# Performance work log

Measured on AMD Instinct MI355X. Metric: run time of the kernel, lower is better.

Reference implementation:

```python
import jax, jax.numpy as jnp
import numpy as np

T, K, H, B = 4096, 64, 128, 128


def setup_inputs() -> dict:
    key = jax.random.key(0)
    ks = jax.random.split(key, 6)
    stdv = 1.0 / np.sqrt(H)  # matches init_weights_random: uniform(-stdv, stdv)
    x = jax.random.normal(ks[0], (T, K, B), dtype=jnp.float32)
    init_hidden_states = jax.random.normal(ks[1], (H, B), dtype=jnp.float32)
    A1 = jax.random.uniform(ks[2], (K, K), minval=-stdv, maxval=stdv, dtype=jnp.float32)
    A2 = jax.random.uniform(ks[3], (K, H), minval=-stdv, maxval=stdv, dtype=jnp.float32)
    A3 = jax.random.uniform(ks[4], (H, K), minval=-stdv, maxval=stdv, dtype=jnp.float32)
    A4 = jax.random.uniform(ks[5], (H, H), minval=-stdv, maxval=stdv, dtype=jnp.float32)
    return {"x": x, "init_hidden_states": init_hidden_states,
            "A1": A1, "A2": A2, "A3": A3, "A4": A4}


def reference(x, init_hidden_states, A1, A2, A3, A4):
    # x: [T, K, B]; hidden: [H, B]
    # known_t = A1 @ x_t + A2 @ h_{t-1};  h_t = A3 @ x_t + A4 @ h_{t-1}
    def step(h, x_t):
        known = A1 @ x_t + A2 @ h
        h_new = A3 @ x_t + A4 @ h
        return h_new, (known, h_new)

    _, (known_seq, hidden_seq) = jax.lax.scan(step, init_hidden_states, x)
    return known_seq, hidden_seq  # [T, K, B], [T, H, B]
```

## Files before the change

kernel.cpp:

```cpp
#include <hip/hip_runtime.h>
#include <stdint.h>

typedef _Float16 half8 __attribute__((ext_vector_type(8)));
typedef float floatx4 __attribute__((ext_vector_type(4)));

constexpr int T  = 4096;
constexpr int KD = 64;
constexpr int HD = 128;
constexpr int BD = 128;
constexpr int KT = KD + HD;
constexpr int CH = 64;
constexpr int LS = T / CH;
constexpr int BC = 32;
constexpr int NSP = BD / BC;

static_assert(CH * LS == T, "");

constexpr size_t W_OFF = 0;
constexpr size_t M_OFF = 73728;
constexpr size_t U_OFF = 131072;
constexpr size_t S_OFF = U_OFF + (size_t)CH * HD * BD * 4;

__device__ __forceinline__ unsigned short f2h(float v) {
  _Float16 h = (_Float16)v;
  return __builtin_bit_cast(unsigned short, h);
}
__device__ __forceinline__ unsigned pack2(float a, float b) {
  return (unsigned)f2h(a) | ((unsigned)f2h(b) << 16);
}
__device__ __forceinline__ int swz(int g, int n) {
  return (g & ~7) | ((g & 7) ^ (n & 7));
}

__global__ __launch_bounds__(256) void prep_kernel(
    const float* __restrict__ A1, const float* __restrict__ A2,
    const float* __restrict__ A3, const float* __restrict__ A4,
    unsigned short* __restrict__ Wf, unsigned short* __restrict__ Mf) {
  if (blockIdx.x < 36) {
    for (int e = 0; e < 4; ++e) {
      int id = blockIdx.x * 1024 + e * 256 + threadIdx.x;
      int r = id / KT, cc = id % KT;
      float v;
      if (r < KD) v = (cc < KD) ? A1[r * KD + cc] : A2[r * HD + (cc - KD)];
      else        v = (cc < KD) ? A3[(r - KD) * KD + cc] : A4[(r - KD) * HD + (cc - KD)];
      Wf[id] = f2h(v);
    }
    return;
  }
  __shared__ __align__(16) unsigned short Mrow[HD * HD];
  __shared__ __align__(16) unsigned short Mcol[HD * HD];
  const int tid = threadIdx.x;
  for (int j = 0; j < 64; ++j) {
    int id = j * 256 + tid;
    int r = id >> 7, cc = id & 127;
    unsigned short hb = f2h(A4[id]);
    Mrow[id] = hb;
    Mcol[cc * HD + r] = hb;
  }
  __syncthreads();
  const int wv = tid >> 6, ln = tid & 63, l15 = ln & 15, q = ln >> 4;
  for (int it = 0; it < 6; ++it) {
    half8 af[2][4];
#pragma unroll
    for (int m = 0; m < 2; ++m)
#pragma unroll
      for (int kt = 0; kt < 4; ++kt)
        af[m][kt] = *reinterpret_cast<const half8*>(
            &Mrow[(wv * 32 + m * 16 + l15) * HD + kt * 32 + q * 8]);
    floatx4 acc[2][8];
#pragma unroll
    for (int m = 0; m < 2; ++m)
#pragma unroll
      for (int nt = 0; nt < 8; ++nt) {
        floatx4 z = {0.f, 0.f, 0.f, 0.f};
        acc[m][nt] = z;
      }
#pragma unroll
    for (int kt = 0; kt < 4; ++kt)
#pragma unroll
      for (int nt = 0; nt < 8; ++nt) {
        half8 bf = *reinterpret_cast<const half8*>(
            &Mcol[(nt * 16 + l15) * HD + kt * 32 + q * 8]);
#pragma unroll
        for (int m = 0; m < 2; ++m)
          acc[m][nt] = __builtin_amdgcn_mfma_f32_16x16x32_f16(af[m][kt], bf, acc[m][nt], 0, 0, 0);
      }
    __syncthreads();
#pragma unroll
    for (int m = 0; m < 2; ++m)
#pragma unroll
      for (int nt = 0; nt < 8; ++nt) {
        int Rb = wv * 32 + m * 16 + q * 4;
        int col = nt * 16 + l15;
#pragma unroll
        for (int r = 0; r < 4; ++r) {
          unsigned short hb = f2h(acc[m][nt][r]);
          Mrow[(Rb + r) * HD + col] = hb;
          Mcol[col * HD + (Rb + r)] = hb;
        }
      }
    __syncthreads();
  }
  for (int j = 0; j < 64; ++j) {
    int id = j * 256 + tid;
    Mf[id] = Mrow[id];
  }
}

template <bool WRITE_OUT, bool ZERO_INIT>
__global__ __launch_bounds__(256) void rnn_pass(
    const float* __restrict__ x, const unsigned short* __restrict__ Wf,
    const float* __restrict__ init_h, const float* __restrict__ s_buf,
    float* __restrict__ u_out, float* __restrict__ out_known,
    float* __restrict__ out_hidden) {
  const int c = blockIdx.x / NSP;
  const int col0 = (blockIdx.x % NSP) * BC;
  const int tid = threadIdx.x;
  const int wv = tid >> 6;
  const int ln = tid & 63;
  const int l15 = ln & 15;
  const int q = ln >> 4;

  __shared__ __align__(16) unsigned short Bsh[BC * KT];

  half8 afrag[3][6];
#pragma unroll
  for (int m = 0; m < 3; ++m)
#pragma unroll
    for (int kt = 0; kt < 6; ++kt)
      afrag[m][kt] = *reinterpret_cast<const half8*>(
          Wf + (wv * 48 + m * 16 + l15) * KT + kt * 32 + q * 8);

  {
    const float* hsrc = nullptr;
    if (!ZERO_INIT) hsrc = (c == 0) ? init_h : (s_buf + (size_t)c * HD * BD);
    int b = tid & 31;
    int r0 = (tid >> 5) * 16;
    float hv[16];
#pragma unroll
    for (int j = 0; j < 16; ++j)
      hv[j] = hsrc ? hsrc[(size_t)(r0 + j) * BD + col0 + b] : 0.f;
#pragma unroll
    for (int hf = 0; hf < 2; ++hf) {
      int o = hf * 8;
      uint4 v;
      v.x = pack2(hv[o + 0], hv[o + 1]);
      v.y = pack2(hv[o + 2], hv[o + 3]);
      v.z = pack2(hv[o + 4], hv[o + 5]);
      v.w = pack2(hv[o + 6], hv[o + 7]);
      int k0 = KD + r0 + o;
      *reinterpret_cast<uint4*>(&Bsh[b * KT + swz(k0 >> 3, b) * 8]) = v;
    }
  }
  {
    int b = tid & 31;
    int k0 = (tid >> 5) * 8;
    const float* xp = x + (size_t)(c * LS) * KD * BD + col0 + b;
    float xv[8];
#pragma unroll
    for (int j = 0; j < 8; ++j) xv[j] = xp[(size_t)(k0 + j) * BD];
    uint4 v;
    v.x = pack2(xv[0], xv[1]);
    v.y = pack2(xv[2], xv[3]);
    v.z = pack2(xv[4], xv[5]);
    v.w = pack2(xv[6], xv[7]);
    *reinterpret_cast<uint4*>(&Bsh[b * KT + swz(k0 >> 3, b) * 8]) = v;
  }
  __syncthreads();

  for (int i = 0; i < LS; ++i) {
    const int t = c * LS + i;
    float xv[8];
    const int b = tid & 31;
    const int xk0 = (tid >> 5) * 8;
    if (i + 1 < LS) {
      const float* xp = x + (size_t)(t + 1) * KD * BD + col0 + b;
#pragma unroll
      for (int j = 0; j < 8; ++j) xv[j] = xp[(size_t)(xk0 + j) * BD];
    }
    floatx4 acc[3][2];
#pragma unroll
    for (int m = 0; m < 3; ++m)
#pragma unroll
      for (int nt = 0; nt < 2; ++nt) {
        floatx4 z = {0.f, 0.f, 0.f, 0.f};
        acc[m][nt] = z;
      }
#pragma unroll
    for (int kt = 0; kt < 6; ++kt)
#pragma unroll
      for (int nt = 0; nt < 2; ++nt) {
        int n = nt * 16 + l15;
        half8 bf = *reinterpret_cast<const half8*>(
            &Bsh[n * KT + swz(kt * 4 + q, n) * 8]);
#pragma unroll
        for (int m = 0; m < 3; ++m)
          acc[m][nt] = __builtin_amdgcn_mfma_f32_16x16x32_f16(
              afrag[m][kt], bf, acc[m][nt], 0, 0, 0);
      }
    __syncthreads();
#pragma unroll
    for (int m = 0; m < 3; ++m) {
      int Rb = wv * 48 + m * 16 + q * 4;
#pragma unroll
      for (int nt = 0; nt < 2; ++nt) {
        int col = col0 + nt * 16 + l15;
        if (Rb < KD) {
          if (WRITE_OUT) {
            float* kp = out_known + (size_t)t * KD * BD + (size_t)Rb * BD + col;
#pragma unroll
            for (int r = 0; r < 4; ++r) kp[(size_t)r * BD] = acc[m][nt][r];
          }
        } else {
          int hr = Rb - KD;
          if (WRITE_OUT) {
            float* hp = out_hidden + (size_t)t * HD * BD + (size_t)hr * BD + col;
#pragma unroll
            for (int r = 0; r < 4; ++r) hp[(size_t)r * BD] = acc[m][nt][r];
          }
          if (!WRITE_OUT && i == LS - 1) {
            float* up = u_out + ((size_t)c * HD + hr) * BD + col;
#pragma unroll
            for (int r = 0; r < 4; ++r) up[(size_t)r * BD] = acc[m][nt][r];
          }
          int n = nt * 16 + l15;
          uint2 pk;
          pk.x = pack2(acc[m][nt][0], acc[m][nt][1]);
          pk.y = pack2(acc[m][nt][2], acc[m][nt][3]);
          *reinterpret_cast<uint2*>(&Bsh[n * KT + swz(Rb >> 3, n) * 8 + (Rb & 7)]) = pk;
        }
      }
    }
    if (i + 1 < LS) {
      uint4 v;
      v.x = pack2(xv[0], xv[1]);
      v.y = pack2(xv[2], xv[3]);
      v.z = pack2(xv[4], xv[5]);
      v.w = pack2(xv[6], xv[7]);
      *reinterpret_cast<uint4*>(&Bsh[b * KT + swz(xk0 >> 3, b) * 8]) = v;
    }
    __syncthreads();
  }
}

__global__ __launch_bounds__(256) void combine_kernel(
    const unsigned short* __restrict__ Mf, const float* __restrict__ init_h,
    const float* __restrict__ u_buf, float* __restrict__ s_buf) {
  const int col0 = blockIdx.x * BC;
  const int tid = threadIdx.x;
  const int wv = tid >> 6;
  const int ln = tid & 63;
  const int l15 = ln & 15;
  const int q = ln >> 4;
  __shared__ __align__(16) unsigned short Hsh[BC * HD];

  half8 af[2][4];
#pragma unroll
  for (int m = 0; m < 2; ++m)
#pragma unroll
    for (int kt = 0; kt < 4; ++kt)
      af[m][kt] = *reinterpret_cast<const half8*>(
          Mf + (wv * 32 + m * 16 + l15) * HD + kt * 32 + q * 8);

  {
    int b = tid & 31;
    int r0 = (tid >> 5) * 16;
    float hv[16];
#pragma unroll
    for (int j = 0; j < 16; ++j)
      hv[j] = init_h[(size_t)(r0 + j) * BD + col0 + b];
#pragma unroll
    for (int hf = 0; hf < 2; ++hf) {
      int o = hf * 8;
      uint4 v;
      v.x = pack2(hv[o + 0], hv[o + 1]);
      v.y = pack2(hv[o + 2], hv[o + 3]);
      v.z = pack2(hv[o + 4], hv[o + 5]);
      v.w = pack2(hv[o + 6], hv[o + 7]);
      *reinterpret_cast<uint4*>(&Hsh[b * HD + swz((r0 + o) >> 3, b) * 8]) = v;
    }
  }
  __syncthreads();

  float ua[2][2][4], ub[2][2][4];
  auto load_u = [&](float(&dst)[2][2][4], int cc) {
    const float* up = u_buf + (size_t)cc * HD * BD;
#pragma unroll
    for (int m = 0; m < 2; ++m) {
      int Rb = wv * 32 + m * 16 + q * 4;
#pragma unroll
      for (int nt = 0; nt < 2; ++nt) {
        int col = col0 + nt * 16 + l15;
#pragma unroll
        for (int r = 0; r < 4; ++r)
          dst[m][nt][r] = up[(size_t)(Rb + r) * BD + col];
      }
    }
  };
  auto stepf = [&](int cc, const float(&uc)[2][2][4]) {
    floatx4 acc[2][2];
#pragma unroll
    for (int m = 0; m < 2; ++m)
#pragma unroll
      for (int nt = 0; nt < 2; ++nt) {
        floatx4 z = {0.f, 0.f, 0.f, 0.f};
        acc[m][nt] = z;
      }
#pragma unroll
    for (int kt = 0; kt < 4; ++kt)
#pragma unroll
      for (int nt = 0; nt < 2; ++nt) {
        int n = nt * 16 + l15;
        half8 bf = *reinterpret_cast<const half8*>(
            &Hsh[n * HD + swz(kt * 4 + q, n) * 8]);
#pragma unroll
        for (int m = 0; m < 2; ++m)
          acc[m][nt] = __builtin_amdgcn_mfma_f32_16x16x32_f16(af[m][kt], bf, acc[m][nt], 0, 0, 0);
      }
    __syncthreads();
#pragma unroll
    for (int m = 0; m < 2; ++m) {
      int Rb = wv * 32 + m * 16 + q * 4;
#pragma unroll
      for (int nt = 0; nt < 2; ++nt) {
        int col = col0 + nt * 16 + l15;
        float s0 = acc[m][nt][0] + uc[m][nt][0];
        float s1 = acc[m][nt][1] + uc[m][nt][1];
        float s2 = acc[m][nt][2] + uc[m][nt][2];
        float s3 = acc[m][nt][3] + uc[m][nt][3];
        float* sp = s_buf + ((size_t)(cc + 1) * HD + Rb) * BD + col;
        sp[0] = s0; sp[BD] = s1; sp[2 * BD] = s2; sp[3 * BD] = s3;
        int n = nt * 16 + l15;
        uint2 pk;
        pk.x = pack2(s0, s1);
        pk.y = pack2(s2, s3);
        *reinterpret_cast<uint2*>(&Hsh[n * HD + swz(Rb >> 3, n) * 8 + (Rb & 7)]) = pk;
      }
    }
    __syncthreads();
  };

  load_u(ua, 0);
  load_u(ub, 1);
  int cc = 0;
  while (cc < CH - 1) {
    stepf(cc, ua);
    if (cc + 2 < CH - 1) load_u(ua, cc + 2);
    ++cc;
    if (cc >= CH - 1) break;
    stepf(cc, ub);
    if (cc + 2 < CH - 1) load_u(ub, cc + 2);
    ++cc;
  }
}

extern "C" void kernel_launch(void* const* d_in, const int* in_sizes, int n_in,
                              void* d_out, int out_size, void* d_ws, size_t ws_size,
                              hipStream_t stream) {
  const float* x  = (const float*)d_in[0];
  const float* ih = (const float*)d_in[1];
  const float* A1 = (const float*)d_in[2];
  const float* A2 = (const float*)d_in[3];
  const float* A3 = (const float*)d_in[4];
  const float* A4 = (const float*)d_in[5];
  char* ws = (char*)d_ws;
  unsigned short* Wf = (unsigned short*)(ws + W_OFF);
  unsigned short* Mf = (unsigned short*)(ws + M_OFF);
  float* u_buf = (float*)(ws + U_OFF);
  float* s_buf = (float*)(ws + S_OFF);
  float* known = (float*)d_out;
  float* hidden = known + (size_t)T * KD * BD;

  prep_kernel<<<37, 256, 0, stream>>>(A1, A2, A3, A4, Wf, Mf);
  rnn_pass<false, true><<<(CH - 1) * NSP, 256, 0, stream>>>(
      x, Wf, nullptr, nullptr, u_buf, nullptr, nullptr);
  combine_kernel<<<NSP, 256, 0, stream>>>(Mf, ih, u_buf, s_buf);
  rnn_pass<true, false><<<CH * NSP, 256, 0, stream>>>(
      x, Wf, ih, s_buf, nullptr, known, hidden);
}
```

Before: 683.7 us.

## Use two-level hierarchical combine with more chunks and fp16 state buffers

Doubles the number of time chunks and replaces the single serial combine over all chunks with a three-stage scheme: grouped aggregation of chunk states, a short serial scan over groups using A4^256, then a parallel fill within groups using A4^32. Chunk-end and start states are stored in fp16 in a batch-major layout, and rnn_pass gets an occupancy hint. This shortens the serial critical path and doubles parallelism in both rnn passes, at the cost of extra kernel launches, higher matrix powers computed in fp16 (accuracy risk), and more rounding of intermediate states.

```diff
diff --git a/kernel.cpp b/kernel.cpp
--- a/kernel.cpp
+++ b/kernel.cpp
@@ -9,22 +9,30 @@
 constexpr int HD = 128;
 constexpr int BD = 128;
 constexpr int KT = KD + HD;
-constexpr int CH = 64;
+constexpr int CH = 128;
 constexpr int LS = T / CH;
 constexpr int BC = 32;
 constexpr int NSP = BD / BC;
+constexpr int G  = 8;
+constexpr int NG = CH / G;
 
 static_assert(CH * LS == T, "");
-
-constexpr size_t W_OFF = 0;
-constexpr size_t M_OFF = 73728;
-constexpr size_t U_OFF = 131072;
-constexpr size_t S_OFF = U_OFF + (size_t)CH * HD * BD * 4;
+static_assert(NG * G == CH, "");
+
+constexpr size_t W_OFF  = 0;
+constexpr size_t M_OFF  = 73728;
+constexpr size_t M8_OFF = M_OFF + 32768;
+constexpr size_t U_OFF  = M8_OFF + 32768;
+constexpr size_t S_OFF  = U_OFF + (size_t)CH * BD * HD * 2;
+constexpr size_t AGG_OFF = S_OFF + (size_t)CH * BD * HD * 2;
 
 __device__ __forceinline__ unsigned short f2h(float v) {
   _Float16 h = (_Float16)v;
   return __builtin_bit_cast(unsigned short, h);
 }
+__device__ __forceinline__ float h2f(unsigned short u) {
+  return (float)__builtin_bit_cast(_Float16, u);
+}
 __device__ __forceinline__ unsigned pack2(float a, float b) {
   return (unsigned)f2h(a) | ((unsigned)f2h(b) << 16);
 }
@@ -35,7 +43,8 @@
 __global__ __launch_bounds__(256) void prep_kernel(
     const float* __restrict__ A1, const float* __restrict__ A2,
     const float* __restrict__ A3, const float* __restrict__ A4,
-    unsigned short* __restrict__ Wf, unsigned short* __restrict__ Mf) {
+    unsigned short* __restrict__ Wf, unsigned short* __restrict__ Mf,
+    unsigned short* __restrict__ M8f) {
   if (blockIdx.x < 36) {
     for (int e = 0; e < 4; ++e) {
       int id = blockIdx.x * 1024 + e * 256 + threadIdx.x;
@@ -59,7 +68,7 @@
   }
   __syncthreads();
   const int wv = tid >> 6, ln = tid & 63, l15 = ln & 15, q = ln >> 4;
-  for (int it = 0; it < 6; ++it) {
+  for (int it = 0; it < 8; ++it) {
     half8 af[2][4];
 #pragma unroll
     for (int m = 0; m < 2; ++m)
@@ -100,18 +109,26 @@
         }
       }
     __syncthreads();
-  }
-  for (int j = 0; j < 64; ++j) {
-    int id = j * 256 + tid;
-    Mf[id] = Mrow[id];
+    if (it == 4) {
+      for (int j = 0; j < 64; ++j) {
+        int id = j * 256 + tid;
+        Mf[id] = Mrow[id];
+      }
+    }
+    if (it == 7) {
+      for (int j = 0; j < 64; ++j) {
+        int id = j * 256 + tid;
+        M8f[id] = Mrow[id];
+      }
+    }
   }
 }
 
 template <bool WRITE_OUT, bool ZERO_INIT>
-__global__ __launch_bounds__(256) void rnn_pass(
+__global__ __launch_bounds__(256, 2) void rnn_pass(
     const float* __restrict__ x, const unsigned short* __restrict__ Wf,
-    const float* __restrict__ init_h, const float* __restrict__ s_buf,
-    float* __restrict__ u_out, float* __restrict__ out_known,
+    const float* __restrict__ init_h, const unsigned short* __restrict__ s16,
+    unsigned short* __restrict__ u16, float* __restrict__ out_known,
     float* __restrict__ out_hidden) {
   const int c = blockIdx.x / NSP;
   const int col0 = (blockIdx.x % NSP) * BC;
@@ -132,24 +149,33 @@
           Wf + (wv * 48 + m * 16 + l15) * KT + kt * 32 + q * 8);
 
   {
-    const float* hsrc = nullptr;
-    if (!ZERO_INIT) hsrc = (c == 0) ? init_h : (s_buf + (size_t)c * HD * BD);
     int b = tid & 31;
     int r0 = (tid >> 5) * 16;
-    float hv[16];
-#pragma unroll
-    for (int j = 0; j < 16; ++j)
-      hv[j] = hsrc ? hsrc[(size_t)(r0 + j) * BD + col0 + b] : 0.f;
-#pragma unroll
-    for (int hf = 0; hf < 2; ++hf) {
-      int o = hf * 8;
-      uint4 v;
-      v.x = pack2(hv[o + 0], hv[o + 1]);
-      v.y = pack2(hv[o + 2], hv[o + 3]);
-      v.z = pack2(hv[o + 4], hv[o + 5]);
-      v.w = pack2(hv[o + 6], hv[o + 7]);
-      int k0 = KD + r0 + o;
-      *reinterpret_cast<uint4*>(&Bsh[b * KT + swz(k0 >> 3, b) * 8]) = v;
+    if (ZERO_INIT) {
+      uint4 z = {0u, 0u, 0u, 0u};
+      *reinterpret_cast<uint4*>(&Bsh[b * KT + swz((KD + r0) >> 3, b) * 8]) = z;
+      *reinterpret_cast<uint4*>(&Bsh[b * KT + swz((KD + r0 + 8) >> 3, b) * 8]) = z;
+    } else if (c == 0) {
+      float hv[16];
+#pragma unroll
+      for (int j = 0; j < 16; ++j)
+        hv[j] = init_h[(size_t)(r0 + j) * BD + col0 + b];
+#pragma unroll
+      for (int hf = 0; hf < 2; ++hf) {
+        int o = hf * 8;
+        uint4 v;
+        v.x = pack2(hv[o + 0], hv[o + 1]);
+        v.y = pack2(hv[o + 2], hv[o + 3]);
+        v.z = pack2(hv[o + 4], hv[o + 5]);
+        v.w = pack2(hv[o + 6], hv[o + 7]);
+        *reinterpret_cast<uint4*>(&Bsh[b * KT + swz((KD + r0 + o) >> 3, b) * 8]) = v;
+      }
+    } else {
+      const unsigned short* sp = s16 + ((size_t)c * BD + col0 + b) * HD + r0;
+      uint4 v0 = *reinterpret_cast<const uint4*>(sp);
+      uint4 v1 = *reinterpret_cast<const uint4*>(sp + 8);
+      *reinterpret_cast<uint4*>(&Bsh[b * KT + swz((KD + r0) >> 3, b) * 8]) = v0;
+      *reinterpret_cast<uint4*>(&Bsh[b * KT + swz((KD + r0 + 8) >> 3, b) * 8]) = v1;
     }
   }
   {
@@ -219,9 +245,11 @@
             for (int r = 0; r < 4; ++r) hp[(size_t)r * BD] = acc[m][nt][r];
           }
           if (!WRITE_OUT && i == LS - 1) {
-            float* up = u_out + ((size_t)c * HD + hr) * BD + col;
-#pragma unroll
-            for (int r = 0; r < 4; ++r) up[(size_t)r * BD] = acc[m][nt][r];
+            unsigned short* up = u16 + ((size_t)c * BD + col) * HD + hr;
+            uint2 pku;
+            pku.x = pack2(acc[m][nt][0], acc[m][nt][1]);
+            pku.y = pack2(acc[m][nt][2], acc[m][nt][3]);
+            *reinterpret_cast<uint2*>(up) = pku;
           }
           int n = nt * 16 + l15;
           uint2 pk;
@@ -243,115 +271,147 @@
   }
 }
 
-__global__ __launch_bounds__(256) void combine_kernel(
-    const unsigned short* __restrict__ Mf, const float* __restrict__ init_h,
-    const float* __restrict__ u_buf, float* __restrict__ s_buf) {
+__device__ __forceinline__ void load_mfrag(const unsigned short* Mp, half8 (&af)[2][4],
+                                           int wv, int l15, int q) {
+#pragma unroll
+  for (int m = 0; m < 2; ++m)
+#pragma unroll
+    for (int kt = 0; kt < 4; ++kt)
+      af[m][kt] = *reinterpret_cast<const half8*>(
+          Mp + (wv * 32 + m * 16 + l15) * HD + kt * 32 + q * 8);
+}
+
+__device__ __forceinline__ void stage_h_f32(const float* __restrict__ hsrc,
+                                            unsigned short* Hsh, int col0, int tid) {
+  int b = tid & 31;
+  int r0 = (tid >> 5) * 16;
+  float hv[16];
+#pragma unroll
+  for (int j = 0; j < 16; ++j)
+    hv[j] = hsrc[(size_t)(r0 + j) * BD + col0 + b];
+#pragma unroll
+  for (int hf = 0; hf < 2; ++hf) {
+    int o = hf * 8;
+    uint4 v;
+    v.x = pack2(hv[o + 0], hv[o + 1]);
+    v.y = pack2(hv[o + 2], hv[o + 3]);
+    v.z = pack2(hv[o + 4], hv[o + 5]);
+    v.w = pack2(hv[o + 6], hv[o + 7]);
+    *reinterpret_cast<uint4*>(&Hsh[b * HD + swz((r0 + o) >> 3, b) * 8]) = v;
+  }
+}
+
+__device__ __forceinline__ void stage_h_f16(const unsigned short* __restrict__ sp16,
+                                            unsigned short* Hsh, int col0, int tid) {
+  int b = tid & 31;
+  int r0 = (tid >> 5) * 16;
+  const unsigned short* sp = sp16 + ((size_t)col0 + b) * HD + r0;
+  uint4 v0 = *reinterpret_cast<const uint4*>(sp);
+  uint4 v1 = *reinterpret_cast<const uint4*>(sp + 8);
+  *reinterpret_cast<uint4*>(&Hsh[b * HD + swz(r0 >> 3, b) * 8]) = v0;
+  *reinterpret_cast<uint4*>(&Hsh[b * HD + swz((r0 + 8) >> 3, b) * 8]) = v1;
+}
+
+template <bool WRITE_S>
+__device__ __forceinline__ void comb_step(
+    const half8 (&af)[2][4], unsigned short* Hsh,
+    const unsigned short* __restrict__ uc, unsigned short* __restrict__ sc,
+    int col0, int wv, int l15, int q) {
+  floatx4 acc[2][2];
+#pragma unroll
+  for (int m = 0; m < 2; ++m)
+#pragma unroll
+    for (int nt = 0; nt < 2; ++nt) {
+      floatx4 z = {0.f, 0.f, 0.f, 0.f};
+      acc[m][nt] = z;
+    }
+#pragma unroll
+  for (int kt = 0; kt < 4; ++kt)
+#pragma unroll
+    for (int nt = 0; nt < 2; ++nt) {
+      int n = nt * 16 + l15;
+      half8 bf = *reinterpret_cast<const half8*>(
+          &Hsh[n * HD + swz(kt * 4 + q, n) * 8]);
+#pragma unroll
+      for (int m = 0; m < 2; ++m)
+        acc[m][nt] = __builtin_amdgcn_mfma_f32_16x16x32_f16(af[m][kt], bf, acc[m][nt], 0, 0, 0);
+    }
+  __syncthreads();
+#pragma unroll
+  for (int m = 0; m < 2; ++m) {
+    int Rb = wv * 32 + m * 16 + q * 4;
+#pragma unroll
+    for (int nt = 0; nt < 2; ++nt) {
+      int col = col0 + nt * 16 + l15;
+      uint2 uv = *reinterpret_cast<const uint2*>(uc + (size_t)col * HD + Rb);
+      float s0 = acc[m][nt][0] + h2f((unsigned short)(uv.x & 0xffff));
+      float s1 = acc[m][nt][1] + h2f((unsigned short)(uv.x >> 16));
+      float s2 = acc[m][nt][2] + h2f((unsigned short)(uv.y & 0xffff));
+      float s3 = acc[m][nt][3] + h2f((unsigned short)(uv.y >> 16));
+      uint2 pk;
+      pk.x = pack2(s0, s1);
+      pk.y = pack2(s2, s3);
+      if (WRITE_S) *reinterpret_cast<uint2*>(sc + (size_t)col * HD + Rb) = pk;
+      int n = nt * 16 + l15;
+      *reinterpret_cast<uint2*>(&Hsh[n * HD + swz(Rb >> 3, n) * 8 + (Rb & 7)]) = pk;
+    }
+  }
+  __syncthreads();
+}
+
+__global__ __launch_bounds__(256) void combine_agg(
+    const unsigned short* __restrict__ Mf, const unsigned short* __restrict__ u16,
+    unsigned short* __restrict__ agg16) {
+  const int j = blockIdx.x / NSP;
+  const int col0 = (blockIdx.x % NSP) * BC;
+  const int tid = threadIdx.x;
+  const int wv = tid >> 6, ln = tid & 63, l15 = ln & 15, q = ln >> 4;
+  __shared__ __align__(16) unsigned short Hsh[BC * HD];
+  half8 af[2][4];
+  load_mfrag(Mf, af, wv, l15, q);
+  for (int jj = tid; jj < BC * HD; jj += 256) Hsh[jj] = 0;
+  __syncthreads();
+  for (int i = 0; i < G; ++i) {
+    const unsigned short* uc = u16 + (size_t)(j * G + i) * BD * HD;
+    if (i == G - 1)
+      comb_step<true>(af, Hsh, uc, agg16 + (size_t)j * BD * HD, col0, wv, l15, q);
+    else
+      comb_step<false>(af, Hsh, uc, nullptr, col0, wv, l15, q);
+  }
+}
+
+__global__ __launch_bounds__(256) void combine_serial(
+    const unsigned short* __restrict__ M8f, const float* __restrict__ init_h,
+    const unsigned short* __restrict__ agg16, unsigned short* __restrict__ s16) {
   const int col0 = blockIdx.x * BC;
   const int tid = threadIdx.x;
-  const int wv = tid >> 6;
-  const int ln = tid & 63;
-  const int l15 = ln & 15;
-  const int q = ln >> 4;
+  const int wv = tid >> 6, ln = tid & 63, l15 = ln & 15, q = ln >> 4;
   __shared__ __align__(16) unsigned short Hsh[BC * HD];
-
   half8 af[2][4];
-#pragma unroll
-  for (int m = 0; m < 2; ++m)
-#pragma unroll
-    for (int kt = 0; kt < 4; ++kt)
-      af[m][kt] = *reinterpret_cast<const half8*>(
-          Mf + (wv * 32 + m * 16 + l15) * HD + kt * 32 + q * 8);
-
-  {
-    int b = tid & 31;
-    int r0 = (tid >> 5) * 16;
-    float hv[16];
-#pragma unroll
-    for (int j = 0; j < 16; ++j)
-      hv[j] = init_h[(size_t)(r0 + j) * BD + col0 + b];
-#pragma unroll
-    for (int hf = 0; hf < 2; ++hf) {
-      int o = hf * 8;
-      uint4 v;
-      v.x = pack2(hv[o + 0], hv[o + 1]);
-      v.y = pack2(hv[o + 2], hv[o + 3]);
-      v.z = pack2(hv[o + 4], hv[o + 5]);
-      v.w = pack2(hv[o + 6], hv[o + 7]);
-      *reinterpret_cast<uint4*>(&Hsh[b * HD + swz((r0 + o) >> 3, b) * 8]) = v;
-    }
-  }
-  __syncthreads();
-
-  float ua[2][2][4], ub[2][2][4];
-  auto load_u = [&](float(&dst)[2][2][4], int cc) {
-    const float* up = u_buf + (size_t)cc * HD * BD;
-#pragma unroll
-    for (int m = 0; m < 2; ++m) {
-      int Rb = wv * 32 + m * 16 + q * 4;
-#pragma unroll
-      for (int nt = 0; nt < 2; ++nt) {
-        int col = col0 + nt * 16 + l15;
-#pragma unroll
-        for (int r = 0; r < 4; ++r)
-          dst[m][nt][r] = up[(size_t)(Rb + r) * BD + col];
-      }
-    }
-  };
-  auto stepf = [&](int cc, const float(&uc)[2][2][4]) {
-    floatx4 acc[2][2];
-#pragma unroll
-    for (int m = 0; m < 2; ++m)
-#pragma unroll
-      for (int nt = 0; nt < 2; ++nt) {
-        floatx4 z = {0.f, 0.f, 0.f, 0.f};
-        acc[m][nt] = z;
-      }
-#pragma unroll
-    for (int kt = 0; kt < 4; ++kt)
-#pragma unroll
-      for (int nt = 0; nt < 2; ++nt) {
-        int n = nt * 16 + l15;
-        half8 bf = *reinterpret_cast<const half8*>(
-            &Hsh[n * HD + swz(kt * 4 + q, n) * 8]);
-#pragma unroll
-        for (int m = 0; m < 2; ++m)
-          acc[m][nt] = __builtin_amdgcn_mfma_f32_16x16x32_f16(af[m][kt], bf, acc[m][nt], 0, 0, 0);
-      }
-    __syncthreads();
-#pragma unroll
-    for (int m = 0; m < 2; ++m) {
-      int Rb = wv * 32 + m * 16 + q * 4;
-#pragma unroll
-      for (int nt = 0; nt < 2; ++nt) {
-        int col = col0 + nt * 16 + l15;
-        float s0 = acc[m][nt][0] + uc[m][nt][0];
-        float s1 = acc[m][nt][1] + uc[m][nt][1];
-        float s2 = acc[m][nt][2] + uc[m][nt][2];
-        float s3 = acc[m][nt][3] + uc[m][nt][3];
-        float* sp = s_buf + ((size_t)(cc + 1) * HD + Rb) * BD + col;
-        sp[0] = s0; sp[BD] = s1; sp[2 * BD] = s2; sp[3 * BD] = s3;
-        int n = nt * 16 + l15;
-        uint2 pk;
-        pk.x = pack2(s0, s1);
-        pk.y = pack2(s2, s3);
-        *reinterpret_cast<uint2*>(&Hsh[n * HD + swz(Rb >> 3, n) * 8 + (Rb & 7)]) = pk;
-      }
-    }
-    __syncthreads();
-  };
-
-  load_u(ua, 0);
-  load_u(ub, 1);
-  int cc = 0;
-  while (cc < CH - 1) {
-    stepf(cc, ua);
-    if (cc + 2 < CH - 1) load_u(ua, cc + 2);
-    ++cc;
-    if (cc >= CH - 1) break;
-    stepf(cc, ub);
-    if (cc + 2 < CH - 1) load_u(ub, cc + 2);
-    ++cc;
-  }
+  load_mfrag(M8f, af, wv, l15, q);
+  stage_h_f32(init_h, Hsh, col0, tid);
+  __syncthreads();
+  for (int j = 0; j < NG - 1; ++j)
+    comb_step<true>(af, Hsh, agg16 + (size_t)j * BD * HD,
+                    s16 + (size_t)(j + 1) * G * BD * HD, col0, wv, l15, q);
+}
+
+__global__ __launch_bounds__(256) void combine_fill(
+    const unsigned short* __restrict__ Mf, const float* __restrict__ init_h,
+    const unsigned short* __restrict__ u16, unsigned short* __restrict__ s16) {
+  const int j = blockIdx.x / NSP;
+  const int col0 = (blockIdx.x % NSP) * BC;
+  const int tid = threadIdx.x;
+  const int wv = tid >> 6, ln = tid & 63, l15 = ln & 15, q = ln >> 4;
+  __shared__ __align__(16) unsigned short Hsh[BC * HD];
+  half8 af[2][4];
+  load_mfrag(Mf, af, wv, l15, q);
+  if (j == 0) stage_h_f32(init_h, Hsh, col0, tid);
+  else        stage_h_f16(s16 + (size_t)j * G * BD * HD, Hsh, col0, tid);
+  __syncthreads();
+  for (int i = 0; i < G - 1; ++i)
+    comb_step<true>(af, Hsh, u16 + (size_t)(j * G + i) * BD * HD,
+                    s16 + (size_t)(j * G + i + 1) * BD * HD, col0, wv, l15, q);
 }
 
 extern "C" void kernel_launch(void* const* d_in, const int* in_sizes, int n_in,
@@ -364,17 +424,21 @@
   const float* A3 = (const float*)d_in[4];
   const float* A4 = (const float*)d_in[5];
   char* ws = (char*)d_ws;
-  unsigned short* Wf = (unsigned short*)(ws + W_OFF);
-  unsigned short* Mf = (unsigned short*)(ws + M_OFF);
-  float* u_buf = (float*)(ws + U_OFF);
-  float* s_buf = (float*)(ws + S_OFF);
+  unsigned short* Wf  = (unsigned short*)(ws + W_OFF);
+  unsigned short* Mf  = (unsigned short*)(ws + M_OFF);
+  unsigned short* M8f = (unsigned short*)(ws + M8_OFF);
+  unsigned short* u16 = (unsigned short*)(ws + U_OFF);
+  unsigned short* s16 = (unsigned short*)(ws + S_OFF);
+  unsigned short* agg16 = (unsigned short*)(ws + AGG_OFF);
   float* known = (float*)d_out;
   float* hidden = known + (size_t)T * KD * BD;
 
-  prep_kernel<<<37, 256, 0, stream>>>(A1, A2, A3, A4, Wf, Mf);
+  prep_kernel<<<37, 256, 0, stream>>>(A1, A2, A3, A4, Wf, Mf, M8f);
   rnn_pass<false, true><<<(CH - 1) * NSP, 256, 0, stream>>>(
-      x, Wf, nullptr, nullptr, u_buf, nullptr, nullptr);
-  combine_kernel<<<NSP, 256, 0, stream>>>(Mf, ih, u_buf, s_buf);
+      x, Wf, nullptr, nullptr, u16, nullptr, nullptr);
+  combine_agg<<<(NG - 1) * NSP, 256, 0, stream>>>(Mf, u16, agg16);
+  combine_serial<<<NSP, 256, 0, stream>>>(M8f, ih, agg16, s16);
+  combine_fill<<<NG * NSP, 256, 0, stream>>>(Mf, ih, u16, s16);
   rnn_pass<true, false><<<CH * NSP, 256, 0, stream>>>(
-      x, Wf, ih, s_buf, nullptr, known, hidden);
-}
+      x, Wf, ih, s16, nullptr, known, hidden);
+}
```

After: 645.4 us. 1.06x faster.
